# Performance work log

Measured on AMD Instinct MI355X. Metric: run time of the kernel, lower is better.

## Reference

```python
import jax, jax.numpy as jnp
import numpy as np

N = 20000      # nodes
E = 320000     # edges (before self loops)
G = 128        # graphs
V = 128        # node-type vocab (VOCAB_SIZE)
DE = 64        # node_emb_dim
H = 4          # heads
C = 128        # hidden_dim per head
D = H * C      # 512, per-layer width
OUT = 256      # output_dim
EPS_LN = 1e-5
NEG_SLOPE = 0.2


def _glorot(k, shape):
    fan_in, fan_out = shape[0], shape[-1]
    s = jnp.sqrt(2.0 / (fan_in + fan_out))
    return jax.random.normal(k, shape, dtype=jnp.float32) * s


def setup_inputs() -> dict:
    key = jax.random.key(0)
    ks = jax.random.split(key, 40)
    inp = {}
    inp['node_ids'] = jax.random.randint(ks[0], (N,), 0, V)
    inp['edge_index'] = jax.random.randint(ks[1], (2, E), 0, N)
    inp['batch_vec'] = jnp.sort(jax.random.randint(ks[2], (N,), 0, G))
    emb = _glorot(ks[3], (V, DE))
    inp['emb'] = emb.at[0].set(0.0)  # padding_idx=0
    in_dims = [DE, D, D, D]
    ki = 4
    for i, di in enumerate(in_dims):
        inp[f'W{i}'] = _glorot(ks[ki], (di, D)); ki += 1
        inp[f'as{i}'] = _glorot(ks[ki], (H, C)); ki += 1
        inp[f'ad{i}'] = _glorot(ks[ki], (H, C)); ki += 1
        inp[f'b{i}'] = jnp.zeros((D,), jnp.float32)
        inp[f'lnw{i}'] = jnp.ones((D,), jnp.float32)
        inp[f'lnb{i}'] = jnp.zeros((D,), jnp.float32)
    inp['res_w0'] = _glorot(ks[ki], (DE, D)); ki += 1
    inp['p1w'] = _glorot(ks[ki], (2 * D, 2 * D)); ki += 1
    inp['p1b'] = jnp.zeros((2 * D,), jnp.float32)
    inp['p2w'] = _glorot(ks[ki], (2 * D, OUT)); ki += 1
    inp['p2b'] = jnp.zeros((OUT,), jnp.float32)
    return inp


def _gat_layer(x, src, dst, W, a_src, a_dst, b):
    # x: [N, din] -> [N, H*C]; edge-softmax attention over incoming edges.
    xp = (x @ W).reshape(N, H, C)
    s_src = (xp * a_src).sum(-1)                      # [N,H]
    s_dst = (xp * a_dst).sum(-1)                      # [N,H]
    e = jax.nn.leaky_relu(s_src[src] + s_dst[dst], NEG_SLOPE)   # [Etot,H]
    emax = jax.ops.segment_max(e, dst, num_segments=N)
    ex = jnp.exp(e - emax[dst])
    denom = jax.ops.segment_sum(ex, dst, num_segments=N)
    alpha = ex / denom[dst]                           # [Etot,H]
    msg = xp[src] * alpha[:, :, None]                 # [Etot,H,C]
    out = jax.ops.segment_sum(msg, dst, num_segments=N)
    return out.reshape(N, D) + b


def _graph_ln(x, batch_vec, w, b):
    # PyG LayerNorm mode='graph': normalize over all nodes+channels per graph.
    Cd = x.shape[-1]
    cnt = jax.ops.segment_sum(jnp.ones((x.shape[0],), x.dtype), batch_vec, num_segments=G) * Cd
    cnt = jnp.maximum(cnt, 1.0)
    mu = jax.ops.segment_sum(x.sum(-1), batch_vec, num_segments=G) / cnt
    xc = x - mu[batch_vec][:, None]
    var = jax.ops.segment_sum((xc * xc).sum(-1), batch_vec, num_segments=G) / cnt
    return xc * jax.lax.rsqrt(var + EPS_LN)[batch_vec][:, None] * w + b


def _forward(emb, W0, as0, ad0, b0, lnw0, lnb0, res_w0,
             W1, as1, ad1, b1, lnw1, lnb1,
             W2, as2, ad2, b2, lnw2, lnb2,
             W3, as3, ad3, b3, lnw3, lnb3,
             p1w, p1b, p2w, p2b, node_ids, edge_index, batch_vec):
    loop = jnp.arange(N)
    src = jnp.concatenate([edge_index[0], loop])  # add_self_loops=True
    dst = jnp.concatenate([edge_index[1], loop])
    x = emb[node_ids]                              # [N,DE]
    layers = [(W0, as0, ad0, b0, lnw0, lnb0), (W1, as1, ad1, b1, lnw1, lnb1),
              (W2, as2, ad2, b2, lnw2, lnb2), (W3, as3, ad3, b3, lnw3, lnb3)]
    for i, (W, asr, adr, b, lnw, lnb) in enumerate(layers):
        residual = x @ res_w0 if i == 0 else x
        x = _gat_layer(x, src, dst, W, asr, adr, b)
        x = _graph_ln(x + residual, batch_vec, lnw, lnb)
    ones = jnp.ones((N,), x.dtype)
    cnt = jnp.maximum(jax.ops.segment_sum(ones, batch_vec, num_segments=G), 1.0)
    mean_pool = jax.ops.segment_sum(x, batch_vec, num_segments=G) / cnt[:, None]
    max_pool = jax.ops.segment_max(x, batch_vec, num_segments=G)
    max_pool = jnp.where(jnp.isfinite(max_pool), max_pool, 0.0)
    h = jnp.concatenate([mean_pool, max_pool], axis=-1)  # [G, 2D]
    h = jax.nn.gelu(h @ p1w + p1b, approximate=False)
    h = h @ p2w + p2b                                     # [G, OUT]
    norm = jnp.maximum(jnp.linalg.norm(h, axis=-1, keepdims=True), 1e-12)
    return h / norm


def reference(node_ids, edge_index, batch_vec, emb,
              W0, as0, ad0, b0, lnw0, lnb0, res_w0,
              W1, as1, ad1, b1, lnw1, lnb1,
              W2, as2, ad2, b2, lnw2, lnb2,
              W3, as3, ad3, b3, lnw3, lnb3,
              p1w, p1b, p2w, p2b):
    return _forward(emb, W0, as0, ad0, b0, lnw0, lnb0, res_w0,
                    W1, as1, ad1, b1, lnw1, lnb1,
                    W2, as2, ad2, b2, lnw2, lnb2,
                    W3, as3, ad3, b3, lnw3, lnb3,
                    p1w, p1b, p2w, p2b, node_ids, edge_index, batch_vec)
```

## Files before the change

### kernel.cpp

```cpp
#include <hip/hip_runtime.h>
#include <hip/hip_fp16.h>
#include <math.h>

constexpr int NN   = 20000;
constexpr int EE   = 320000;
constexpr int ET   = EE + NN;
constexpr int GG   = 128;
constexpr int DEE  = 64;
constexpr int DD   = 512;
constexpr int OUTD = 256;

using half8 = __attribute__((ext_vector_type(8))) _Float16;
using f32x4 = __attribute__((ext_vector_type(4))) float;

__device__ __forceinline__ void ldg2lds16(const void* g, void* l) {
  __builtin_amdgcn_global_load_lds((const __attribute__((address_space(1))) unsigned*)g,
                                   (__attribute__((address_space(3))) unsigned*)l, 16, 0, 0);
}

__global__ __launch_bounds__(256) void k_embf16(const int* __restrict__ ids,
                                                const float* __restrict__ emb,
                                                __half* __restrict__ x0) {
  for (int i = blockIdx.x * 256 + threadIdx.x; i < NN * 16; i += gridDim.x * 256) {
    int n = i >> 4, q = (i & 15) * 4;
    float4 v = *(const float4*)(emb + (size_t)ids[n] * DEE + q);
    __half2* o = (__half2*)(x0 + (size_t)n * DEE + q);
    o[0] = __floats2half2_rn(v.x, v.y);
    o[1] = __floats2half2_rn(v.z, v.w);
  }
}

__global__ __launch_bounds__(256) void k_wT16(const float* __restrict__ W,
                                              __half* __restrict__ Th,
                                              int K, int N) {
  __shared__ float t[32][33];
  int n0 = blockIdx.x * 32, k0 = blockIdx.y * 32;
  int c = threadIdx.x & 31, r4 = threadIdx.x >> 5;
  for (int rr = 0; rr < 32; rr += 8)
    t[rr + r4][c] = W[(size_t)(k0 + rr + r4) * N + n0 + c];
  __syncthreads();
  for (int rr = 0; rr < 32; rr += 8) {
    int n = n0 + rr + r4, k = k0 + c;
    Th[(size_t)n * K + k] = __float2half_rn(t[c][rr + r4]);
  }
}

__global__ __launch_bounds__(256) void k_count(const int* __restrict__ ei, int* __restrict__ cnt) {
  for (int k = blockIdx.x * 256 + threadIdx.x; k < ET; k += gridDim.x * 256) {
    int d = (k < EE) ? ei[EE + k] : (k - EE);
    atomicAdd(&cnt[d], 1);
  }
}

__global__ __launch_bounds__(1024) void k_scan(const int* __restrict__ cnt, int* __restrict__ off) {
  __shared__ int part[1024];
  int tid = threadIdx.x;
  constexpr int CH = (NN + 1023) / 1024;
  int base = tid * CH;
  int s = 0;
  for (int i = 0; i < CH; ++i) { int idx = base + i; if (idx < NN) s += cnt[idx]; }
  part[tid] = s;
  __syncthreads();
  for (int o = 1; o < 1024; o <<= 1) {
    int add = (tid >= o) ? part[tid - o] : 0;
    int v = part[tid];
    __syncthreads();
    part[tid] = v + add;
    __syncthreads();
  }
  int run = (tid == 0) ? 0 : part[tid - 1];
  for (int i = 0; i < CH; ++i) {
    int idx = base + i;
    if (idx < NN) { off[idx] = run; run += cnt[idx]; }
  }
  if (tid == 1023) off[NN] = ET;
}

__global__ __launch_bounds__(256) void k_scatter(const int* __restrict__ ei, const int* __restrict__ off,
                                                 int* __restrict__ cur, int* __restrict__ csrc) {
  for (int k = blockIdx.x * 256 + threadIdx.x; k < ET; k += gridDim.x * 256) {
    int s = (k < EE) ? ei[k]      : (k - EE);
    int d = (k < EE) ? ei[EE + k] : (k - EE);
    int p = atomicAdd(&cur[d], 1);
    csrc[off[d] + p] = s;
  }
}

template<int DOTS>
__global__ __launch_bounds__(256) void k_mfma3(const __half* __restrict__ A,
                                               const __half* __restrict__ Bh,
                                               __half* __restrict__ C,
                                               int M, int K, int NC,
                                               const float* __restrict__ asw,
                                               const float* __restrict__ adw,
                                               float* __restrict__ sspS,
                                               float* __restrict__ sspD) {
  __shared__ __half lds[2 * 128 * 64];
  __half* As  = lds;
  __half* Bhs = lds + 8192;
  const int tid = threadIdx.x, l = tid & 63, w = tid >> 6;
  const int wr = w >> 1, wc = w & 1;
  const int m0 = blockIdx.y * 128, n0 = blockIdx.x * 128;
  const int l15 = l & 15, l16 = l >> 4;
  const int sr = l >> 3;
  const int ss = (l & 7) ^ sr;

  float a_s[4], a_d[4];
  if (DOTS) {
#pragma unroll
    for (int j = 0; j < 4; ++j) {
      int col = n0 + wc * 64 + j * 16 + l15;
      a_s[j] = asw[col];
      a_d[j] = adw[col];
    }
  }

  f32x4 acc[4][4] = {};
  for (int k0 = 0; k0 < K; k0 += 64) {
#pragma unroll
    for (int j = 0; j < 4; ++j) {
      int rbase = j * 32 + w * 8;
      int rl = rbase + sr;
      int gA = min(m0 + rl, M - 1);
      int gB = n0 + rl;
      const size_t ko = (size_t)(k0 + ss * 8);
      ldg2lds16(A  + (size_t)gA * K + ko, As  + rbase * 64);
      ldg2lds16(Bh + (size_t)gB * K + ko, Bhs + rbase * 64);
    }
    __syncthreads();
#pragma unroll
    for (int kh = 0; kh < 2; ++kh) {
      half8 af[4], bhf[4];
#pragma unroll
      for (int t = 0; t < 4; ++t) {
        int ra = wr * 64 + t * 16 + l15;
        int ca = (kh * 4 + l16) ^ (ra & 7);
        af[t] = *(const half8*)(As + ra * 64 + ca * 8);
        int rb = wc * 64 + t * 16 + l15;
        int cb = (kh * 4 + l16) ^ (rb & 7);
        bhf[t] = *(const half8*)(Bhs + rb * 64 + cb * 8);
      }
#pragma unroll
      for (int i = 0; i < 4; ++i)
#pragma unroll
        for (int j = 0; j < 4; ++j)
          acc[i][j] = __builtin_amdgcn_mfma_f32_16x16x32_f16(af[i], bhf[j], acc[i][j], 0, 0, 0);
    }
    __syncthreads();
  }
  const int hh = n0 >> 7;
#pragma unroll
  for (int i = 0; i < 4; ++i) {
#pragma unroll
    for (int r = 0; r < 4; ++r) {
      int row = m0 + wr * 64 + i * 16 + l16 * 4 + r;
      if (DOTS) {
        float vs = 0.f, vd = 0.f;
#pragma unroll
        for (int j = 0; j < 4; ++j) {
          vs = fmaf(acc[i][j][r], a_s[j], vs);
          vd = fmaf(acc[i][j][r], a_d[j], vd);
        }
#pragma unroll
        for (int o = 1; o < 16; o <<= 1) { vs += __shfl_xor(vs, o); vd += __shfl_xor(vd, o); }
        if (l15 == 0 && row < M) {
          sspS[(size_t)wc * (NN * 4) + row * 4 + hh] = vs;
          sspD[(size_t)wc * (NN * 4) + row * 4 + hh] = vd;
        }
      }
      if (row >= M) continue;
#pragma unroll
      for (int j = 0; j < 4; ++j) {
        int col = n0 + wc * 64 + j * 16 + l15;
        C[(size_t)row * NC + col] = __float2half(acc[i][j][r]);
      }
    }
  }
}

__global__ __launch_bounds__(256) void k_scomb(const float* __restrict__ sspS,
                                               const float* __restrict__ sspD,
                                               float* __restrict__ ssrc,
                                               float* __restrict__ sdst) {
  int idx = blockIdx.x * 256 + threadIdx.x;
  if (idx < NN * 4) {
    ssrc[idx] = sspS[idx] + sspS[NN * 4 + idx];
    sdst[idx] = sspD[idx] + sspD[NN * 4 + idx];
  }
}

__global__ __launch_bounds__(256) void k_mfmaK(const __half* __restrict__ A,
                                               const __half* __restrict__ Bh,
                                               float* __restrict__ part,
                                               int M, int K, int NC, int Kc) {
  __shared__ __half lds[2 * 128 * 64];
  __half* As  = lds;
  __half* Bhs = lds + 8192;
  const int tid = threadIdx.x, l = tid & 63, w = tid >> 6;
  const int wr = w >> 1, wc = w & 1;
  const int m0 = blockIdx.y * 128, n0 = blockIdx.x * 128;
  const int kz = blockIdx.z;
  const int kb = kz * Kc, ke = kb + Kc;
  const int l15 = l & 15, l16 = l >> 4;
  const int sr = l >> 3;
  const int ss = (l & 7) ^ sr;

  f32x4 acc[4][4] = {};
  for (int k0 = kb; k0 < ke; k0 += 64) {
#pragma unroll
    for (int j = 0; j < 4; ++j) {
      int rbase = j * 32 + w * 8;
      int rl = rbase + sr;
      int gA = min(m0 + rl, M - 1);
      int gB = n0 + rl;
      const size_t ko = (size_t)(k0 + ss * 8);
      ldg2lds16(A  + (size_t)gA * K + ko, As  + rbase * 64);
      ldg2lds16(Bh + (size_t)gB * K + ko, Bhs + rbase * 64);
    }
    __syncthreads();
#pragma unroll
    for (int kh = 0; kh < 2; ++kh) {
      half8 af[4], bhf[4];
#pragma unroll
      for (int t = 0; t < 4; ++t) {
        int ra = wr * 64 + t * 16 + l15;
        int ca = (kh * 4 + l16) ^ (ra & 7);
        af[t] = *(const half8*)(As + ra * 64 + ca * 8);
        int rb = wc * 64 + t * 16 + l15;
        int cb = (kh * 4 + l16) ^ (rb & 7);
        bhf[t] = *(const half8*)(Bhs + rb * 64 + cb * 8);
      }
#pragma unroll
      for (int i = 0; i < 4; ++i)
#pragma unroll
        for (int j = 0; j < 4; ++j)
          acc[i][j] = __builtin_amdgcn_mfma_f32_16x16x32_f16(af[i], bhf[j], acc[i][j], 0, 0, 0);
    }
    __syncthreads();
  }
  float* pz = part + (size_t)kz * M * NC;
#pragma unroll
  for (int i = 0; i < 4; ++i) {
#pragma unroll
    for (int r = 0; r < 4; ++r) {
      int row = m0 + wr * 64 + i * 16 + l16 * 4 + r;
      if (row >= M) continue;
#pragma unroll
      for (int j = 0; j < 4; ++j) {
        int col = n0 + wc * 64 + j * 16 + l15;
        pz[(size_t)row * NC + col] = acc[i][j][r];
      }
    }
  }
}

__global__ __launch_bounds__(256) void k_fin_gelu(const float* __restrict__ part,
                                                  const float* __restrict__ bias,
                                                  __half* __restrict__ outh) {
  int idx = blockIdx.x * 256 + threadIdx.x;
  if (idx >= GG * 1024) return;
  int c = idx & 1023;
  float v = bias[c];
#pragma unroll
  for (int z = 0; z < 8; ++z) v += part[(size_t)z * GG * 1024 + idx];
  v = 0.5f * v * (1.0f + erff(v * 0.70710678118654752f));
  outh[idx] = __float2half_rn(v);
}

__global__ __launch_bounds__(256) void k_fin_l2(const float* __restrict__ part,
                                                const float* __restrict__ bias,
                                                float* __restrict__ out) {
  int g = blockIdx.x, t = threadIdx.x;
  float v = bias[t];
#pragma unroll
  for (int z = 0; z < 8; ++z) v += part[(size_t)z * GG * OUTD + g * OUTD + t];
  float q = v * v;
#pragma unroll
  for (int o = 32; o; o >>= 1) q += __shfl_xor(q, o);
  __shared__ float w[4];
  int wv = t >> 6, ln = t & 63;
  if (ln == 0) w[wv] = q;
  __syncthreads();
  float tot = w[0] + w[1] + w[2] + w[3];
  float nrm = fmaxf(sqrtf(tot), 1e-12f);
  out[(size_t)g * OUTD + t] = v / nrm;
}

__global__ __launch_bounds__(256) void k_eweight(const float* __restrict__ ssrc,
                                                 const float* __restrict__ sdst,
                                                 const int* __restrict__ off,
                                                 const int* __restrict__ csr,
                                                 int2* __restrict__ ewk) {
  int wv = threadIdx.x >> 6, ln = threadIdx.x & 63;
  int n = blockIdx.x * 4 + wv;
  int beg = off[n], end = off[n + 1];
  float4 sd4 = *(const float4*)(sdst + (size_t)n * 4);
  float4 wreg[2];
  int    skreg[2];
  float d0 = 0.f, d1 = 0.f, d2 = 0.f, d3 = 0.f;
  int cnt = 0;
  for (int k = beg + ln; k < end; k += 64) {
    int sk = csr[k];
    float4 s = *(const float4*)(ssrc + (size_t)sk * 4);
    float e0 = s.x + sd4.x; e0 = (e0 > 0.f) ? e0 : 0.2f * e0;
    float e1 = s.y + sd4.y; e1 = (e1 > 0.f) ? e1 : 0.2f * e1;
    float e2 = s.z + sd4.z; e2 = (e2 > 0.f) ? e2 : 0.2f * e2;
    float e3 = s.w + sd4.w; e3 = (e3 > 0.f) ? e3 : 0.2f * e3;
    float4 wv4 = make_float4(__expf(e0), __expf(e1), __expf(e2), __expf(e3));
    if (cnt < 2) { wreg[cnt] = wv4; skreg[cnt] = sk; }
    ++cnt;
    d0 += wv4.x; d1 += wv4.y; d2 += wv4.z; d3 += wv4.w;
  }
#pragma unroll
  for (int o = 32; o; o >>= 1) {
    d0 += __shfl_xor(d0, o); d1 += __shfl_xor(d1, o);
    d2 += __shfl_xor(d2, o); d3 += __shfl_xor(d3, o);
  }
  float r0 = 1.0f / d0, r1 = 1.0f / d1, r2 = 1.0f / d2, r3 = 1.0f / d3;
  cnt = 0;
  for (int k = beg + ln; k < end; k += 64) {
    float4 wv4;
    int sk;
    if (cnt < 2) { wv4 = wreg[cnt]; sk = skreg[cnt]; }
    else {
      sk = csr[k];
      float4 s = *(const float4*)(ssrc + (size_t)sk * 4);
      float e0 = s.x + sd4.x; e0 = (e0 > 0.f) ? e0 : 0.2f * e0;
      float e1 = s.y + sd4.y; e1 = (e1 > 0.f) ? e1 : 0.2f * e1;
      float e2 = s.z + sd4.z; e2 = (e2 > 0.f) ? e2 : 0.2f * e2;
      float e3 = s.w + sd4.w; e3 = (e3 > 0.f) ? e3 : 0.2f * e3;
      wv4 = make_float4(__expf(e0), __expf(e1), __expf(e2), __expf(e3));
    }
    ++cnt;
    ewk[k]          = make_int2(sk, __float_as_int(wv4.x * r0));
    ewk[ET + k]     = make_int2(sk, __float_as_int(wv4.y * r1));
    ewk[2 * ET + k] = make_int2(sk, __float_as_int(wv4.z * r2));
    ewk[3 * ET + k] = make_int2(sk, __float_as_int(wv4.w * r3));
  }
}

__global__ __launch_bounds__(256, 8) void k_aggc(const __half* __restrict__ xp16,
                                                 const int2* __restrict__ ewk,
                                                 const int* __restrict__ off,
                                                 const float* __restrict__ bias,
                                                 __half* __restrict__ xio,
                                                 float* __restrict__ psq) {
  const int bid = blockIdx.x;
  const int cb = bid & 7;
  const int chunk = bid >> 3;
  const int wv = threadIdx.x >> 6, l = threadIdx.x & 63;
  const int g = l >> 3, q = l & 7;
  const int h = cb >> 1;
  const int n = __builtin_amdgcn_readfirstlane(chunk * 4 + wv);
  const int beg = off[n], end = off[n + 1];
  const int2* __restrict__ ewh = ewk + (size_t)h * ET;
  const __half* __restrict__ xb = xp16 + cb * 64;
  const unsigned qoff = (unsigned)q * 16;

  uint4 rres = *(const uint4*)(xio + (size_t)n * DD + cb * 64 + q * 8);
  float4 bi0 = *(const float4*)(bias + cb * 64 + q * 8);
  float4 bi1 = *(const float4*)(bias + cb * 64 + q * 8 + 4);

  float acc[8] = {};
  for (int k = beg; k < end; k += 8) {
    int e = k + g;
    int i = min(e, end - 1);
    int2 rec = ewh[i];
    float w = __int_as_float(rec.y);
    w = (e < end) ? w : 0.f;
    unsigned boff = ((unsigned)rec.x << 10) | qoff;
    uint4 r = *(const uint4*)((const char*)xb + boff);
    const __half2* hp = (const __half2*)&r;
#pragma unroll
    for (int j = 0; j < 4; ++j) {
      float2 f = __half22float2(hp[j]);
      acc[2 * j]     = fmaf(w, f.x, acc[2 * j]);
      acc[2 * j + 1] = fmaf(w, f.y, acc[2 * j + 1]);
    }
  }
#pragma unroll
  for (int j = 0; j < 8; ++j) {
    acc[j] += __shfl_xor(acc[j], 8);
    acc[j] += __shfl_xor(acc[j], 16);
    acc[j] += __shfl_xor(acc[j], 32);
  }
  const __half2* rp = (const __half2*)&rres;
  float biv[8] = {bi0.x, bi0.y, bi0.z, bi0.w, bi1.x, bi1.y, bi1.z, bi1.w};
  float o[8];
  float ps = 0.f, pq = 0.f;
#pragma unroll
  for (int j = 0; j < 4; ++j) {
    float2 f = __half22float2(rp[j]);
    o[2 * j]     = acc[2 * j]     + biv[2 * j]     + f.x;
    o[2 * j + 1] = acc[2 * j + 1] + biv[2 * j + 1] + f.y;
    ps += o[2 * j] + o[2 * j + 1];
    pq += o[2 * j] * o[2 * j] + o[2 * j + 1] * o[2 * j + 1];
  }
  if (g == 0) {
    uint4 st; __half2* sp = (__half2*)&st;
#pragma unroll
    for (int j = 0; j < 4; ++j) sp[j] = __floats2half2_rn(o[2 * j], o[2 * j + 1]);
    *(uint4*)(xio + (size_t)n * DD + cb * 64 + q * 8) = st;
  }
#pragma unroll
  for (int o2 = 1; o2 < 8; o2 <<= 1) { ps += __shfl_xor(ps, o2); pq += __shfl_xor(pq, o2); }
  if (l == 0) {
    psq[(size_t)n * 16 + cb * 2]     = ps;
    psq[(size_t)n * 16 + cb * 2 + 1] = pq;
  }
}

__device__ __forceinline__ int lowb(const int* a, int n, int key) {
  int lo = 0, hi = n;
  while (lo < hi) { int mid = (lo + hi) >> 1; if (a[mid] < key) lo = mid + 1; else hi = mid; }
  return lo;
}

__global__ __launch_bounds__(256) void k_stats2(const float* __restrict__ psq,
                                                const int* __restrict__ batch,
                                                float* __restrict__ gmu, float* __restrict__ grstd) {
  int g = blockIdx.x, tid = threadIdx.x;
  __shared__ int sb, se;
  __shared__ float rs[4], rq[4];
  if (tid == 0) { sb = lowb(batch, NN, g); se = lowb(batch, NN, g + 1); }
  __syncthreads();
  int b = sb, e = se;
  float ps = 0.f, pq = 0.f;
  for (int n = b + tid; n < e; n += 256) {
    const float4* p = (const float4*)(psq + (size_t)n * 16);
#pragma unroll
    for (int i = 0; i < 4; ++i) {
      float4 v = p[i];
      ps += v.x + v.z;
      pq += v.y + v.w;
    }
  }
#pragma unroll
  for (int o = 32; o; o >>= 1) { ps += __shfl_xor(ps, o); pq += __shfl_xor(pq, o); }
  int wv = tid >> 6, ln = tid & 63;
  if (ln == 0) { rs[wv] = ps; rq[wv] = pq; }
  __syncthreads();
  if (tid == 0) {
    float S = rs[0] + rs[1] + rs[2] + rs[3];
    float Q = rq[0] + rq[1] + rq[2] + rq[3];
    float cnt = fmaxf((float)(e - b) * (float)DD, 1.0f);
    float mu  = S / cnt;
    float var = fmaxf(Q / cnt - mu * mu, 0.0f);
    gmu[g]   = mu;
    grstd[g] = rsqrtf(var + 1e-5f);
  }
}

__global__ __launch_bounds__(256) void k_norm(__half* __restrict__ x, const int* __restrict__ batch,
                                              const float* __restrict__ gmu, const float* __restrict__ grstd,
                                              const float* __restrict__ lnw, const float* __restrict__ lnb) {
  for (int i8 = blockIdx.x * 256 + threadIdx.x; i8 < NN * DD / 8; i8 += gridDim.x * 256) {
    int i = i8 * 8;
    int n = i >> 9, d = i & 511;
    int g = batch[n];
    float mu = gmu[g], rs = grstd[g];
    uint4 raw = *(uint4*)(x + i);
    __half2* hp = (__half2*)&raw;
    float4 w0 = *(const float4*)(lnw + d);
    float4 w1 = *(const float4*)(lnw + d + 4);
    float4 b0 = *(const float4*)(lnb + d);
    float4 b1 = *(const float4*)(lnb + d + 4);
    float wv[8] = {w0.x,w0.y,w0.z,w0.w,w1.x,w1.y,w1.z,w1.w};
    float bv[8] = {b0.x,b0.y,b0.z,b0.w,b1.x,b1.y,b1.z,b1.w};
#pragma unroll
    for (int j = 0; j < 4; ++j) {
      float2 f = __half22float2(hp[j]);
      f.x = (f.x - mu) * rs * wv[2*j]   + bv[2*j];
      f.y = (f.y - mu) * rs * wv[2*j+1] + bv[2*j+1];
      hp[j] = __floats2half2_rn(f.x, f.y);
    }
    *(uint4*)(x + i) = raw;
  }
}

__global__ __launch_bounds__(256) void k_pool(const __half* __restrict__ x, const int* __restrict__ batch,
                                              __half* __restrict__ pool16) {
  int g = blockIdx.x, tid = threadIdx.x;
  __shared__ int sb, se;
  if (tid == 0) { sb = lowb(batch, NN, g); se = lowb(batch, NN, g + 1); }
  __syncthreads();
  int b = sb, e = se;
  float s0 = 0.f, s1 = 0.f, m0 = -INFINITY, m1 = -INFINITY;
  for (int n = b; n < e; ++n) {
    float v0 = __half2float(x[(size_t)n * DD + tid]);
    float v1 = __half2float(x[(size_t)n * DD + tid + 256]);
    s0 += v0; s1 += v1;
    m0 = fmaxf(m0, v0); m1 = fmaxf(m1, v1);
  }
  int cnt = e - b;
  float inv = 1.0f / (float)(cnt > 0 ? cnt : 1);
  pool16[(size_t)g * 1024 + tid]             = __float2half_rn(s0 * inv);
  pool16[(size_t)g * 1024 + tid + 256]       = __float2half_rn(s1 * inv);
  pool16[(size_t)g * 1024 + 512 + tid]       = __float2half_rn((cnt > 0) ? m0 : 0.f);
  pool16[(size_t)g * 1024 + 512 + tid + 256] = __float2half_rn((cnt > 0) ? m1 : 0.f);
}

extern "C" void kernel_launch(void* const* d_in, const int* in_sizes, int n_in,
                              void* d_out, int out_size, void* d_ws, size_t ws_size,
                              hipStream_t stream) {
  const int*   node_ids = (const int*)d_in[0];
  const int*   ei       = (const int*)d_in[1];
  const int*   batch    = (const int*)d_in[2];
  const float* emb      = (const float*)d_in[3];
  const float* W[4]  = {(const float*)d_in[4],  (const float*)d_in[10], (const float*)d_in[16], (const float*)d_in[22]};
  const float* AS[4] = {(const float*)d_in[5],  (const float*)d_in[11], (const float*)d_in[17], (const float*)d_in[23]};
  const float* AD[4] = {(const float*)d_in[6],  (const float*)d_in[12], (const float*)d_in[18], (const float*)d_in[24]};
  const float* BV[4] = {(const float*)d_in[7],  (const float*)d_in[13], (const float*)d_in[19], (const float*)d_in[25]};
  const float* LW[4] = {(const float*)d_in[8],  (const float*)d_in[14], (const float*)d_in[20], (const float*)d_in[26]};
  const float* LB[4] = {(const float*)d_in[9],  (const float*)d_in[15], (const float*)d_in[21], (const float*)d_in[27]};
  const float* res_w0 = (const float*)d_in[28];
  const float* p1w    = (const float*)d_in[29];
  const float* p1b    = (const float*)d_in[30];
  const float* p2w    = (const float*)d_in[31];
  const float* p2b    = (const float*)d_in[32];
  float* out = (float*)d_out;

  char* ws = (char*)d_ws;
  size_t pos = 0;
  auto alloc = [&](size_t bytes) -> char* {
    char* p = ws + pos;
    pos = (pos + bytes + 255) & ~size_t(255);
    return p;
  };
  __half* xr16  = (__half*)alloc((size_t)NN * DD * 2);
  __half* xp16  = (__half*)alloc((size_t)NN * DD * 2);
  __half* x0f   = (__half*)alloc((size_t)NN * DEE * 2);
  float*  ssrc  = (float*)alloc((size_t)NN * 4 * 4);
  float*  sdst  = (float*)alloc((size_t)NN * 4 * 4);
  float*  sspS  = (float*)alloc((size_t)2 * NN * 4 * 4);
  float*  sspD  = (float*)alloc((size_t)2 * NN * 4 * 4);
  int*    coff  = (int*)alloc((size_t)(NN + 1) * 4);
  int*    ccur  = (int*)alloc((size_t)NN * 4);
  int*    csrc  = (int*)alloc((size_t)ET * 4);
  int2*   ewk   = (int2*)alloc((size_t)ET * 4 * 8);
  float*  psq   = (float*)alloc((size_t)NN * 16 * 4);
  float*  gmu   = (float*)alloc((size_t)GG * 4 * 2);
  float*  grstd = gmu + GG;
  __half* w0t = (__half*)alloc((size_t)DEE * DD * 2);
  __half* rwt = (__half*)alloc((size_t)DEE * DD * 2);
  __half* wt[4] = {w0t, nullptr, nullptr, nullptr};
  for (int i = 1; i < 4; ++i) wt[i] = (__half*)alloc((size_t)DD * DD * 2);
  __half* p1t = (__half*)alloc((size_t)1024 * 1024 * 2);
  __half* p2t = (__half*)alloc((size_t)OUTD * 1024 * 2);
  __half* pool16 = (__half*)alloc((size_t)GG * 1024 * 2);
  __half* h1_16  = (__half*)alloc((size_t)GG * 1024 * 2);
  float*  part1  = (float*)alloc((size_t)8 * GG * 1024 * 4);
  float*  part2  = (float*)alloc((size_t)8 * GG * OUTD * 4);
  (void)ws_size; (void)in_sizes; (void)n_in; (void)out_size;

  hipMemsetAsync(ccur, 0, (size_t)NN * 4, stream);
  k_embf16<<<1250, 256, 0, stream>>>(node_ids, emb, x0f);
  k_count<<<1024, 256, 0, stream>>>(ei, ccur);
  k_scan<<<1, 1024, 0, stream>>>(ccur, coff);
  hipMemsetAsync(ccur, 0, (size_t)NN * 4, stream);
  k_scatter<<<1024, 256, 0, stream>>>(ei, coff, ccur, csrc);
  k_wT16<<<dim3(16, 2),  256, 0, stream>>>(W[0],   w0t, DEE, DD);
  k_wT16<<<dim3(16, 2),  256, 0, stream>>>(res_w0, rwt, DEE, DD);
  for (int i = 1; i < 4; ++i)
    k_wT16<<<dim3(16, 16), 256, 0, stream>>>(W[i], wt[i], DD, DD);
  k_wT16<<<dim3(32, 32), 256, 0, stream>>>(p1w, p1t, 1024, 1024);
  k_wT16<<<dim3(8, 32),  256, 0, stream>>>(p2w, p2t, 1024, OUTD);

  k_mfma3<1><<<dim3(4, 157), 256, 0, stream>>>(x0f, w0t, xp16, NN, DEE, DD,
                                               AS[0], AD[0], sspS, sspD);
  k_mfma3<0><<<dim3(4, 157), 256, 0, stream>>>(x0f, rwt, xr16, NN, DEE, DD,
                                               nullptr, nullptr, nullptr, nullptr);
  k_scomb<<<(NN * 4 + 255) / 256, 256, 0, stream>>>(sspS, sspD, ssrc, sdst);

  for (int L = 0; L < 4; ++L) {
    k_eweight<<<NN / 4, 256, 0, stream>>>(ssrc, sdst, coff, csrc, ewk);
    k_aggc<<<NN * 2, 256, 0, stream>>>(xp16, ewk, coff, BV[L], xr16, psq);
    k_stats2<<<GG, 256, 0, stream>>>(psq, batch, gmu, grstd);
    k_norm<<<2048, 256, 0, stream>>>(xr16, batch, gmu, grstd, LW[L], LB[L]);
    if (L < 3) {
      k_mfma3<1><<<dim3(4, 157), 256, 0, stream>>>(xr16, wt[L + 1], xp16, NN, DD, DD,
                                                   AS[L + 1], AD[L + 1], sspS, sspD);
      k_scomb<<<(NN * 4 + 255) / 256, 256, 0, stream>>>(sspS, sspD, ssrc, sdst);
    }
  }

  k_pool<<<GG, 256, 0, stream>>>(xr16, batch, pool16);
  k_mfmaK<<<dim3(8, 1, 8), 256, 0, stream>>>(pool16, p1t, part1, GG, 1024, 1024, 128);
  k_fin_gelu<<<512, 256, 0, stream>>>(part1, p1b, h1_16);
  k_mfmaK<<<dim3(2, 1, 8), 256, 0, stream>>>(h1_16, p2t, part2, GG, 1024, OUTD, 128);
  k_fin_l2<<<GG, 256, 0, stream>>>(part2, p2b, out);
}
```

Baseline: 636.6 us.

## Pack edge records into 32-bit with fp16 weight and pipeline aggregation loads

Edge records shrink from an int2 (source index plus fp32 weight) to one 32-bit word holding a 16-bit source index and an fp16 attention weight. This halves edge-record traffic in both the weight and aggregation kernels. The aggregation loop now uses inline v_fma_mix_f32 to multiply fp16 weights by fp16 features with fp32 accumulation, drops the explicit conversions, and unrolls the first 32 edges with software-pipelined record prefetch. Risks: the attention weights lose precision in fp16, and the 16-bit source field only holds indices below 65536, which the 20000 nodes satisfy.

```diff
diff --git a/kernel.cpp b/kernel.cpp
--- a/kernel.cpp
+++ b/kernel.cpp
@@ -290,7 +290,7 @@
                                                  const float* __restrict__ sdst,
                                                  const int* __restrict__ off,
                                                  const int* __restrict__ csr,
-                                                 int2* __restrict__ ewk) {
+                                                 unsigned* __restrict__ ewk) {
   int wv = threadIdx.x >> 6, ln = threadIdx.x & 63;
   int n = blockIdx.x * 4 + wv;
   int beg = off[n], end = off[n + 1];
@@ -332,15 +332,27 @@
       wv4 = make_float4(__expf(e0), __expf(e1), __expf(e2), __expf(e3));
     }
     ++cnt;
-    ewk[k]          = make_int2(sk, __float_as_int(wv4.x * r0));
-    ewk[ET + k]     = make_int2(sk, __float_as_int(wv4.y * r1));
-    ewk[2 * ET + k] = make_int2(sk, __float_as_int(wv4.z * r2));
-    ewk[3 * ET + k] = make_int2(sk, __float_as_int(wv4.w * r3));
-  }
+    unsigned sh = (unsigned)sk << 16;
+    ewk[k]          = sh | (unsigned)__half_as_ushort(__float2half_rn(wv4.x * r0));
+    ewk[ET + k]     = sh | (unsigned)__half_as_ushort(__float2half_rn(wv4.y * r1));
+    ewk[2 * ET + k] = sh | (unsigned)__half_as_ushort(__float2half_rn(wv4.z * r2));
+    ewk[3 * ET + k] = sh | (unsigned)__half_as_ushort(__float2half_rn(wv4.w * r3));
+  }
+}
+
+__device__ __forceinline__ void accmix(float* acc, unsigned rec, const uint4& x) {
+  asm("v_fma_mix_f32 %0, %1, %2, %0 op_sel:[0,0,0] op_sel_hi:[1,1,0]" : "+v"(acc[0]) : "v"(rec), "v"(x.x));
+  asm("v_fma_mix_f32 %0, %1, %2, %0 op_sel:[0,1,0] op_sel_hi:[1,1,0]" : "+v"(acc[1]) : "v"(rec), "v"(x.x));
+  asm("v_fma_mix_f32 %0, %1, %2, %0 op_sel:[0,0,0] op_sel_hi:[1,1,0]" : "+v"(acc[2]) : "v"(rec), "v"(x.y));
+  asm("v_fma_mix_f32 %0, %1, %2, %0 op_sel:[0,1,0] op_sel_hi:[1,1,0]" : "+v"(acc[3]) : "v"(rec), "v"(x.y));
+  asm("v_fma_mix_f32 %0, %1, %2, %0 op_sel:[0,0,0] op_sel_hi:[1,1,0]" : "+v"(acc[4]) : "v"(rec), "v"(x.z));
+  asm("v_fma_mix_f32 %0, %1, %2, %0 op_sel:[0,1,0] op_sel_hi:[1,1,0]" : "+v"(acc[5]) : "v"(rec), "v"(x.z));
+  asm("v_fma_mix_f32 %0, %1, %2, %0 op_sel:[0,0,0] op_sel_hi:[1,1,0]" : "+v"(acc[6]) : "v"(rec), "v"(x.w));
+  asm("v_fma_mix_f32 %0, %1, %2, %0 op_sel:[0,1,0] op_sel_hi:[1,1,0]" : "+v"(acc[7]) : "v"(rec), "v"(x.w));
 }
 
 __global__ __launch_bounds__(256, 8) void k_aggc(const __half* __restrict__ xp16,
-                                                 const int2* __restrict__ ewk,
+                                                 const unsigned* __restrict__ ewk,
                                                  const int* __restrict__ off,
                                                  const float* __restrict__ bias,
                                                  __half* __restrict__ xio,
@@ -353,7 +365,7 @@
   const int h = cb >> 1;
   const int n = __builtin_amdgcn_readfirstlane(chunk * 4 + wv);
   const int beg = off[n], end = off[n + 1];
-  const int2* __restrict__ ewh = ewk + (size_t)h * ET;
+  const unsigned* __restrict__ ewh = ewk + (size_t)h * ET;
   const __half* __restrict__ xb = xp16 + cb * 64;
   const unsigned qoff = (unsigned)q * 16;
 
@@ -362,21 +374,39 @@
   float4 bi1 = *(const float4*)(bias + cb * 64 + q * 8 + 4);
 
   float acc[8] = {};
-  for (int k = beg; k < end; k += 8) {
-    int e = k + g;
-    int i = min(e, end - 1);
-    int2 rec = ewh[i];
-    float w = __int_as_float(rec.y);
-    w = (e < end) ? w : 0.f;
-    unsigned boff = ((unsigned)rec.x << 10) | qoff;
-    uint4 r = *(const uint4*)((const char*)xb + boff);
-    const __half2* hp = (const __half2*)&r;
-#pragma unroll
-    for (int j = 0; j < 4; ++j) {
-      float2 f = __half22float2(hp[j]);
-      acc[2 * j]     = fmaf(w, f.x, acc[2 * j]);
-      acc[2 * j + 1] = fmaf(w, f.y, acc[2 * j + 1]);
-    }
+  {
+    int e0 = beg + g, e1 = beg + 8 + g, e2 = beg + 16 + g, e3 = beg + 24 + g;
+    unsigned rA = ewh[min(e0, end - 1)];
+    unsigned rB = ewh[min(e1, end - 1)];
+    unsigned rC = ewh[min(e2, end - 1)];
+    unsigned rD = ewh[min(e3, end - 1)];
+    rA = (e0 < end) ? rA : 0u;
+    rB = (e1 < end) ? rB : 0u;
+    rC = (e2 < end) ? rC : 0u;
+    rD = (e3 < end) ? rD : 0u;
+    uint4 xA = *(const uint4*)((const char*)xb + (((rA >> 6) & 0xFFFFFC00u) | qoff));
+    uint4 xB = *(const uint4*)((const char*)xb + (((rB >> 6) & 0xFFFFFC00u) | qoff));
+    uint4 xC = *(const uint4*)((const char*)xb + (((rC >> 6) & 0xFFFFFC00u) | qoff));
+    uint4 xD = *(const uint4*)((const char*)xb + (((rD >> 6) & 0xFFFFFC00u) | qoff));
+    accmix(acc, rA, xA);
+    accmix(acc, rB, xB);
+    accmix(acc, rC, xC);
+    accmix(acc, rD, xD);
+  }
+  if (beg + 32 < end) {
+    int k = beg + 32;
+    unsigned rA = ewh[min(k + g, end - 1)];
+    unsigned rB = ewh[min(k + 8 + g, end - 1)];
+    for (; k + 8 < end; k += 8) {
+      rA = ((k + g) < end) ? rA : 0u;
+      uint4 xA = *(const uint4*)((const char*)xb + (((rA >> 6) & 0xFFFFFC00u) | qoff));
+      unsigned rN = ewh[min(k + 16 + g, end - 1)];
+      accmix(acc, rA, xA);
+      rA = rB; rB = rN;
+    }
+    rA = ((k + g) < end) ? rA : 0u;
+    uint4 xA = *(const uint4*)((const char*)xb + (((rA >> 6) & 0xFFFFFC00u) | qoff));
+    accmix(acc, rA, xA);
   }
 #pragma unroll
   for (int j = 0; j < 8; ++j) {
@@ -537,7 +567,7 @@
   int*    coff  = (int*)alloc((size_t)(NN + 1) * 4);
   int*    ccur  = (int*)alloc((size_t)NN * 4);
   int*    csrc  = (int*)alloc((size_t)ET * 4);
-  int2*   ewk   = (int2*)alloc((size_t)ET * 4 * 8);
+  unsigned* ewk = (unsigned*)alloc((size_t)ET * 4 * 4);
   float*  psq   = (float*)alloc((size_t)NN * 16 * 4);
   float*  gmu   = (float*)alloc((size_t)GG * 4 * 2);
   float*  grstd = gmu + GG;
```

Measured after the change: 583.1 us. 8.4% less time.
